# Performance work log

Measured on AMD Instinct MI355X. Metric: run time of the kernel, lower is better.

The kernel has to match this reference:

```python
import jax, jax.numpy as jnp
import numpy as np

N = 16384      # nodes
E = 524288     # edges (avg degree 32)
F_IN = 128     # input features
H1 = 256       # first_gcn_dimensions
H2 = 256       # second_gcn_dimensions
D1 = 64        # first_dense_neurons
D2 = 2         # second_dense_neurons (fixed by EYE=ones(2))


def setup_inputs() -> dict:
    key = jax.random.key(0)
    ks = jax.random.split(key, 8)
    w = lambda k, shp: (jax.random.normal(k, shp, jnp.float32) * 0.05)
    return dict(
        features=jax.random.normal(ks[0], (N, F_IN), jnp.float32),
        edges=jax.random.randint(ks[1], (2, E), 0, N),
        W1=w(ks[2], (F_IN, H1)), b1=jnp.zeros((H1,), jnp.float32),
        W2=w(ks[3], (H1, H2)), b2=jnp.zeros((H2,), jnp.float32),
        fc1_w=w(ks[4], (D1, H2)), fc1_b=jnp.zeros((D1,), jnp.float32),
        fc2_w=w(ks[5], (D2, D1)), fc2_b=jnp.zeros((D2,), jnp.float32),
    )


def gcn_conv(x, W, b, src, dst, n):
    """PyG GCNConv: xW, add self-loops, symmetric D^-1/2 (A+I) D^-1/2 aggregation."""
    x = x @ W
    loops = jnp.arange(n)
    s = jnp.concatenate([src, loops])
    d = jnp.concatenate([dst, loops])
    deg = jax.ops.segment_sum(jnp.ones(s.shape, x.dtype), d, num_segments=n)
    dinv = jnp.where(deg > 0, jax.lax.rsqrt(deg), 0.0)
    msg = x[s] * (dinv[s] * dinv[d])[:, None]          # gather + scale
    return jax.ops.segment_sum(msg, d, num_segments=n) + b  # scatter-add


def reference(features, edges, W1, b1, W2, b2, fc1_w, fc1_b, fc2_w, fc2_b):
    n = features.shape[0]
    src, dst = edges[0], edges[1]
    h1 = jax.nn.relu(gcn_conv(features, W1, b1, src, dst, n))
    h2 = gcn_conv(h1, W2, b2, src, dst, n)                 # [N, H2]
    a1 = jnp.tanh(h2 @ fc1_w.T + fc1_b)                    # [N, D1]
    assignment = jax.nn.softmax(a1 @ fc2_w.T + fc2_b, axis=1)  # [N, 2]
    group_features = assignment.T @ h2                     # [2, H2]
    # to_dense_adj: dense NxN adjacency, duplicate edges accumulate
    adj = jnp.zeros((n, n), h2.dtype).at[src, dst].add(1.0)
    new_adj = assignment.T @ (adj @ assignment)            # [2, 2]
    positive = jnp.clip(group_features[0][None, :], -100.0, 100.0)
    negative = jnp.clip(group_features[1][None, :], -100.0, 100.0)
    # F.normalize(p=1, dim=1) with eps=1e-12
    denom = jnp.maximum(jnp.sum(jnp.abs(new_adj), axis=1, keepdims=True), 1e-12)
    norm_diag = jnp.diag(new_adj / denom)
    pos_penalty = jnp.mean((norm_diag - 1.0) ** 2)         # MSE vs ones(2)
    graph_embedding = jnp.mean(group_features, axis=0, keepdims=True)  # [1, H2]
    return (graph_embedding, positive, negative, pos_penalty)
```

## Files before the change

### kernel.cpp

```cpp
#include <hip/hip_runtime.h>
#include <hip/hip_bf16.h>
#include <math.h>

#define N_NODES 16384
#define N_EDGES 524288
#define F_IN 128
#define H1 256
#define H2 256
#define D1 64
#define NA_GRID 128
#define DEG_CAP 96

typedef __attribute__((ext_vector_type(8))) short short8;
typedef __attribute__((ext_vector_type(4))) float floatx4;
typedef unsigned short ushort_t;
typedef unsigned int uint_t;

__device__ inline float bf2f(ushort_t u) {
    union { uint_t i; float f; } v;
    v.i = ((uint_t)u) << 16;
    return v.f;
}
__device__ inline ushort_t f2bs(float x) {
    __hip_bfloat16 h = __float2bfloat16(x);
    return *reinterpret_cast<ushort_t*>(&h);
}

__global__ __launch_bounds__(256) void prep_fill(
    const int* __restrict__ src, const int* __restrict__ dst,
    const float* __restrict__ features, const float* __restrict__ W1,
    const float* __restrict__ W2, const float* __restrict__ fc1_w,
    int* __restrict__ cur, int* __restrict__ col, ushort_t* __restrict__ z,
    ushort_t* __restrict__ W1t, ushort_t* __restrict__ W2t,
    ushort_t* __restrict__ fc1bf) {
    int b = blockIdx.x, t = threadIdx.x;
    if (b < 2048) {
        int e = b * 256 + t;
        int d = dst[e];
        int pos = atomicAdd(&cur[d], 1);
        if (pos < DEG_CAP) col[d * DEG_CAP + pos] = src[e];
    } else if (b < 4096) {
        int idx = ((b - 2048) * 256 + t) * 4;
        float4 v = *(const float4*)&features[idx];
        uint2 p;
        p.x = (uint_t)f2bs(v.x) | ((uint_t)f2bs(v.y) << 16);
        p.y = (uint_t)f2bs(v.z) | ((uint_t)f2bs(v.w) << 16);
        *(uint2*)&z[idx] = p;
    } else if (b < 4224) {
        int idx = (b - 4096) * 256 + t;
        int n = idx >> 7, k = idx & 127;
        W1t[idx] = f2bs(W1[k * 256 + n]);
    } else if (b < 4480) {
        int idx = (b - 4224) * 256 + t;
        int n = idx >> 8, k = idx & 255;
        W2t[idx] = f2bs(W2[k * 256 + n]);
    } else {
        int idx = (b - 4480) * 256 + t;
        fc1bf[idx] = f2bs(fc1_w[idx]);
    }
}

__global__ __launch_bounds__(256) void fused_layer1(
    const ushort_t* __restrict__ zfeat, const int* __restrict__ cnt,
    const int* __restrict__ col, const float* __restrict__ b1,
    const ushort_t* __restrict__ W1t, const ushort_t* __restrict__ W2t,
    ushort_t* __restrict__ bufY) {
    __shared__ __align__(16) ushort_t Az[16 * 136];
    __shared__ __align__(16) ushort_t Ah[16 * 264];
    const int tid = threadIdx.x;
    const int lane = tid & 63;
    const int wave = tid >> 6;
    const int m = lane & 15;
    const int quad = lane >> 4;
    const int row0 = blockIdx.x * 16;

    for (int ii = 0; ii < 4; ++ii) {
        const int nl = wave * 4 + ii;
        const int node = __builtin_amdgcn_readfirstlane(row0 + nl);
        const int foff = lane * 2;
        const int deg = cnt[node];
        float dnode = rsqrtf((float)(deg + 1));
        uint_t self = *(const uint_t*)&zfeat[(size_t)node * 128 + foff];
        float a0 = dnode * bf2f((ushort_t)(self & 0xffff));
        float a1 = dnode * bf2f((ushort_t)(self >> 16));
        const int s0 = node * DEG_CAP;
        const int s1 = s0 + min(deg, DEG_CAP);
        int base = s0;
        for (; base + 8 <= s1; base += 8) {
            uint_t uu[8]; float dv[8];
            #pragma unroll
            for (int q = 0; q < 8; ++q) {
                int j = col[base + q];
                dv[q] = rsqrtf((float)(cnt[j] + 1));
                uu[q] = *(const uint_t*)&zfeat[(size_t)j * 128 + foff];
            }
            #pragma unroll
            for (int q = 0; q < 8; ++q) {
                a0 += dv[q] * bf2f((ushort_t)(uu[q] & 0xffff));
                a1 += dv[q] * bf2f((ushort_t)(uu[q] >> 16));
            }
        }
        for (; base < s1; ++base) {
            int j = col[base];
            float dv = rsqrtf((float)(cnt[j] + 1));
            uint_t u = *(const uint_t*)&zfeat[(size_t)j * 128 + foff];
            a0 += dv * bf2f((ushort_t)(u & 0xffff));
            a1 += dv * bf2f((ushort_t)(u >> 16));
        }
        *(uint_t*)&Az[nl * 136 + foff] =
            (uint_t)f2bs(a0 * dnode) | ((uint_t)f2bs(a1 * dnode) << 16);
    }
    __syncthreads();

    const int wcol0 = wave * 64;
    floatx4 acc[4];
    const floatx4 zero4 = {0.f, 0.f, 0.f, 0.f};
    #pragma unroll
    for (int j = 0; j < 4; ++j) acc[j] = zero4;
    #pragma unroll
    for (int k0 = 0; k0 < 128; k0 += 32) {
        short8 a = *(const short8*)&Az[m * 136 + k0 + quad * 8];
        #pragma unroll
        for (int j = 0; j < 4; ++j) {
            short8 bb = *(const short8*)
                &W1t[(size_t)(wcol0 + j * 16 + m) * 128 + k0 + quad * 8];
            acc[j] = __builtin_amdgcn_mfma_f32_16x16x32_bf16(a, bb, acc[j], 0, 0, 0);
        }
    }
    #pragma unroll
    for (int j = 0; j < 4; ++j) {
        int cg = wcol0 + j * 16 + m;
        float bv = b1[cg];
        #pragma unroll
        for (int r = 0; r < 4; ++r) {
            float v = fmaxf(acc[j][r] + bv, 0.0f);
            Ah[(quad * 4 + r) * 264 + cg] = f2bs(v);
        }
    }
    __syncthreads();

    #pragma unroll
    for (int j = 0; j < 4; ++j) acc[j] = zero4;
    #pragma unroll
    for (int k0 = 0; k0 < 256; k0 += 32) {
        short8 a = *(const short8*)&Ah[m * 264 + k0 + quad * 8];
        #pragma unroll
        for (int j = 0; j < 4; ++j) {
            short8 bb = *(const short8*)
                &W2t[(size_t)(wcol0 + j * 16 + m) * 256 + k0 + quad * 8];
            acc[j] = __builtin_amdgcn_mfma_f32_16x16x32_bf16(a, bb, acc[j], 0, 0, 0);
        }
    }
    float rs4[4];
    #pragma unroll
    for (int r = 0; r < 4; ++r)
        rs4[r] = rsqrtf((float)(cnt[row0 + quad * 4 + r] + 1));
    #pragma unroll
    for (int j = 0; j < 4; ++j) {
        int cg = wcol0 + j * 16 + m;
        #pragma unroll
        for (int r = 0; r < 4; ++r)
            bufY[(size_t)(row0 + quad * 4 + r) * 256 + cg] = f2bs(acc[j][r] * rs4[r]);
    }
}

__global__ __launch_bounds__(256) void fused_assign(
    const ushort_t* __restrict__ bufY, const int* __restrict__ cnt,
    const int* __restrict__ col, const float* __restrict__ b2,
    const ushort_t* __restrict__ fc1bf, const float* __restrict__ fc1_b,
    const float* __restrict__ fc2_w, const float* __restrict__ fc2_b,
    float* __restrict__ assign, float* __restrict__ gfr) {
    __shared__ __align__(16) ushort_t Ah[16 * 264];
    __shared__ float sha[16][65];
    __shared__ float sas0[16], sas1[16];
    const int tid = threadIdx.x;
    const int lane = tid & 63;
    const int wave = tid >> 6;
    const int m = lane & 15;
    const int quad = lane >> 4;
    const int row0 = blockIdx.x * 16;

    for (int ii = 0; ii < 4; ++ii) {
        const int nl = wave * 4 + ii;
        const int node = __builtin_amdgcn_readfirstlane(row0 + nl);
        const int foff = lane * 4;
        const int deg = cnt[node];
        float a0, a1, a2, a3;
        {
            uint2 u = *(const uint2*)&bufY[(size_t)node * 256 + foff];
            a0 = bf2f((ushort_t)(u.x & 0xffff));
            a1 = bf2f((ushort_t)(u.x >> 16));
            a2 = bf2f((ushort_t)(u.y & 0xffff));
            a3 = bf2f((ushort_t)(u.y >> 16));
        }
        const int s0 = node * DEG_CAP;
        const int s1 = s0 + min(deg, DEG_CAP);
        int base = s0;
        for (; base + 8 <= s1; base += 8) {
            uint2 uu[8];
            #pragma unroll
            for (int q = 0; q < 8; ++q) {
                int j = col[base + q];
                uu[q] = *(const uint2*)&bufY[(size_t)j * 256 + foff];
            }
            #pragma unroll
            for (int q = 0; q < 8; ++q) {
                a0 += bf2f((ushort_t)(uu[q].x & 0xffff));
                a1 += bf2f((ushort_t)(uu[q].x >> 16));
                a2 += bf2f((ushort_t)(uu[q].y & 0xffff));
                a3 += bf2f((ushort_t)(uu[q].y >> 16));
            }
        }
        for (; base < s1; ++base) {
            int j = col[base];
            uint2 u = *(const uint2*)&bufY[(size_t)j * 256 + foff];
            a0 += bf2f((ushort_t)(u.x & 0xffff));
            a1 += bf2f((ushort_t)(u.x >> 16));
            a2 += bf2f((ushort_t)(u.y & 0xffff));
            a3 += bf2f((ushort_t)(u.y >> 16));
        }
        float di = rsqrtf((float)(deg + 1));
        uint2 pk;
        pk.x = (uint_t)f2bs(a0 * di + b2[foff + 0]) |
               ((uint_t)f2bs(a1 * di + b2[foff + 1]) << 16);
        pk.y = (uint_t)f2bs(a2 * di + b2[foff + 2]) |
               ((uint_t)f2bs(a3 * di + b2[foff + 3]) << 16);
        *(uint2*)&Ah[nl * 264 + foff] = pk;
    }
    __syncthreads();

    floatx4 acc = {0.f, 0.f, 0.f, 0.f};
    #pragma unroll
    for (int k0 = 0; k0 < 256; k0 += 32) {
        short8 a = *(const short8*)&Ah[m * 264 + k0 + quad * 8];
        short8 bb = *(const short8*)
            &fc1bf[(size_t)(wave * 16 + m) * 256 + k0 + quad * 8];
        acc = __builtin_amdgcn_mfma_f32_16x16x32_bf16(a, bb, acc, 0, 0, 0);
    }
    {
        int cg = wave * 16 + m;
        float bv = fc1_b[cg];
        #pragma unroll
        for (int r = 0; r < 4; ++r)
            sha[quad * 4 + r][cg] = tanhf(acc[r] + bv);
    }
    __syncthreads();

    if (tid < 16) {
        float p0 = fc2_b[0], p1 = fc2_b[1];
        #pragma unroll 8
        for (int t = 0; t < 64; ++t) {
            float a = sha[tid][t];
            p0 += a * fc2_w[t];
            p1 += a * fc2_w[64 + t];
        }
        float mx = fmaxf(p0, p1);
        float e0 = expf(p0 - mx), e1 = expf(p1 - mx);
        float inv = 1.0f / (e0 + e1);
        float2 as; as.x = e0 * inv; as.y = e1 * inv;
        *(float2*)&assign[(row0 + tid) * 2] = as;
        sas0[tid] = as.x; sas1[tid] = as.y;
    }
    __syncthreads();

    float acc0 = 0.f, acc1 = 0.f;
    #pragma unroll
    for (int i = 0; i < 16; ++i) {
        float h = bf2f(Ah[i * 264 + tid]);
        acc0 += sas0[i] * h;
        acc1 += sas1[i] * h;
    }
    float* gfc = gfr + (blockIdx.x & 3) * 512;
    atomicAdd(&gfc[tid], acc0);
    atomicAdd(&gfc[256 + tid], acc1);
}

__global__ __launch_bounds__(256) void newadj_fin(
    const int* __restrict__ src, const int* __restrict__ dst,
    const float* __restrict__ assign, float* __restrict__ napart,
    int* __restrict__ cntt, const float* __restrict__ gfr,
    float* __restrict__ out) {
    __shared__ float red[4][4];
    __shared__ int sticket;
    const int tid = threadIdx.x;
    const int b = blockIdx.x;
    const int lane = tid & 63;
    const int wave = tid >> 6;

    float a00 = 0.f, a01 = 0.f, a10 = 0.f, a11 = 0.f;
    for (int e = b * 256 + tid; e < N_EDGES; e += NA_GRID * 256) {
        int s = src[e], d = dst[e];
        float s0 = assign[s * 2], s1 = assign[s * 2 + 1];
        float d0 = assign[d * 2], d1 = assign[d * 2 + 1];
        a00 += s0 * d0; a01 += s0 * d1; a10 += s1 * d0; a11 += s1 * d1;
    }
    #pragma unroll
    for (int off = 32; off; off >>= 1) {
        a00 += __shfl_down(a00, off);
        a01 += __shfl_down(a01, off);
        a10 += __shfl_down(a10, off);
        a11 += __shfl_down(a11, off);
    }
    if (lane == 0) {
        red[wave][0] = a00; red[wave][1] = a01;
        red[wave][2] = a10; red[wave][3] = a11;
    }
    __syncthreads();
    if (tid < 4) {
        float v = red[0][tid] + red[1][tid] + red[2][tid] + red[3][tid];
        __hip_atomic_store(&napart[b * 4 + tid], v, __ATOMIC_RELEASE,
                           __HIP_MEMORY_SCOPE_AGENT);
    }
    __syncthreads();
    if (tid == 0)
        sticket = __hip_atomic_fetch_add(cntt, 1, __ATOMIC_ACQ_REL,
                                         __HIP_MEMORY_SCOPE_AGENT);
    __syncthreads();
    if (sticket != NA_GRID - 1) return;

    float acc = 0.f;
    for (int i = lane; i < NA_GRID; i += 64)
        acc += __hip_atomic_load(&napart[i * 4 + wave], __ATOMIC_RELAXED,
                                 __HIP_MEMORY_SCOPE_AGENT);
    #pragma unroll
    for (int off = 32; off; off >>= 1) acc += __shfl_down(acc, off);
    __shared__ float na[4];
    if (lane == 0) na[wave] = acc;
    __syncthreads();
    float g0 = gfr[tid] + gfr[512 + tid] + gfr[1024 + tid] + gfr[1536 + tid];
    float g1 = gfr[256 + tid] + gfr[768 + tid] + gfr[1280 + tid] + gfr[1792 + tid];
    out[tid] = 0.5f * (g0 + g1);
    out[256 + tid] = fminf(fmaxf(g0, -100.f), 100.f);
    out[512 + tid] = fminf(fmaxf(g1, -100.f), 100.f);
    if (tid == 0) {
        float n00 = na[0], n01 = na[1], n10 = na[2], n11 = na[3];
        float den0 = fmaxf(fabsf(n00) + fabsf(n01), 1e-12f);
        float den1 = fmaxf(fabsf(n10) + fabsf(n11), 1e-12f);
        float x0 = n00 / den0 - 1.0f;
        float x1 = n11 / den1 - 1.0f;
        out[768] = 0.5f * (x0 * x0 + x1 * x1);
    }
}


extern "C" void kernel_launch(void* const* d_in, const int* in_sizes, int n_in,
                              void* d_out, int out_size, void* d_ws, size_t ws_size,
                              hipStream_t stream) {
    const float* features = (const float*)d_in[0];
    const int* edges = (const int*)d_in[1];
    const int* src = edges;
    const int* dst = edges + N_EDGES;
    const float* W1 = (const float*)d_in[2];
    const float* b1 = (const float*)d_in[3];
    const float* W2 = (const float*)d_in[4];
    const float* b2 = (const float*)d_in[5];
    const float* fc1_w = (const float*)d_in[6];
    const float* fc1_b = (const float*)d_in[7];
    const float* fc2_w = (const float*)d_in[8];
    const float* fc2_b = (const float*)d_in[9];
    float* out = (float*)d_out;

    char* ws = (char*)d_ws;
    auto carve = [&](size_t bytes) {
        void* q = (void*)ws;
        ws += (bytes + 255) & ~(size_t)255;
        return q;
    };
    int* cur = (int*)carve(N_NODES * 4);
    float* gfr = (float*)carve(4 * 512 * 4);
    int* cnt_na = (int*)carve(256);
    int* col = (int*)carve((size_t)N_NODES * DEG_CAP * 4);
    float* assign = (float*)carve(N_NODES * 2 * 4);
    float* napart = (float*)carve(NA_GRID * 4 * 4);
    ushort_t* fc1bf = (ushort_t*)carve(64 * 256 * 2);
    ushort_t* zfeat = (ushort_t*)carve((size_t)N_NODES * F_IN * 2);
    ushort_t* W1t = (ushort_t*)carve(256 * 128 * 2);
    ushort_t* W2t = (ushort_t*)carve(256 * 256 * 2);
    ushort_t* bufY = (ushort_t*)carve((size_t)N_NODES * 256 * 2);

    hipMemsetAsync(cur, 0, N_NODES * 4 + 4 * 512 * 4 + 256, stream);

    prep_fill<<<4544, 256, 0, stream>>>(src, dst, features, W1, W2, fc1_w,
                                        cur, col, zfeat, W1t, W2t, fc1bf);
    fused_layer1<<<N_NODES / 16, 256, 0, stream>>>(
        zfeat, cur, col, b1, W1t, W2t, bufY);
    fused_assign<<<N_NODES / 16, 256, 0, stream>>>(
        bufY, cur, col, b2, fc1bf, fc1_b, fc2_w, fc2_b, assign, gfr);
    newadj_fin<<<NA_GRID, 256, 0, stream>>>(src, dst, assign, napart,
                                            cnt_na, gfr, out);
}
```

Measured before the change: 206.3 us.

## Pre-scale features by source degree and widen fused blocks to 512 threads

Adds a separate kernel that converts features to bf16 already multiplied by each node's D^-1/2, after degree counts are known. This removes the per-neighbor cnt[j] load and rsqrt from the layer-1 gather loop. Both fused kernels now run 512-thread blocks (8 waves, 2 nodes per wave), which halves the MFMA column tiles per wave, and the bf16 unpack uses a mask instead of a shift. The cost is an extra kernel launch and a serialization point: feature conversion can no longer overlap with the edge fill inside prep_fill.

After: 189.6 us. 8.1% less time.

```diff
diff --git a/kernel.cpp b/kernel.cpp
--- a/kernel.cpp
+++ b/kernel.cpp
@@ -21,6 +21,16 @@
     v.i = ((uint_t)u) << 16;
     return v.f;
 }
+__device__ inline float u2f_lo(uint_t u) {
+    union { uint_t i; float f; } v;
+    v.i = u << 16;
+    return v.f;
+}
+__device__ inline float u2f_hi(uint_t u) {
+    union { uint_t i; float f; } v;
+    v.i = u & 0xffff0000u;
+    return v.f;
+}
 __device__ inline ushort_t f2bs(float x) {
     __hip_bfloat16 h = __float2bfloat16(x);
     return *reinterpret_cast<ushort_t*>(&h);
@@ -28,9 +38,9 @@
 
 __global__ __launch_bounds__(256) void prep_fill(
     const int* __restrict__ src, const int* __restrict__ dst,
-    const float* __restrict__ features, const float* __restrict__ W1,
-    const float* __restrict__ W2, const float* __restrict__ fc1_w,
-    int* __restrict__ cur, int* __restrict__ col, ushort_t* __restrict__ z,
+    const float* __restrict__ W1, const float* __restrict__ W2,
+    const float* __restrict__ fc1_w,
+    int* __restrict__ cur, int* __restrict__ col,
     ushort_t* __restrict__ W1t, ushort_t* __restrict__ W2t,
     ushort_t* __restrict__ fc1bf) {
     int b = blockIdx.x, t = threadIdx.x;
@@ -39,29 +49,35 @@
         int d = dst[e];
         int pos = atomicAdd(&cur[d], 1);
         if (pos < DEG_CAP) col[d * DEG_CAP + pos] = src[e];
-    } else if (b < 4096) {
-        int idx = ((b - 2048) * 256 + t) * 4;
-        float4 v = *(const float4*)&features[idx];
-        uint2 p;
-        p.x = (uint_t)f2bs(v.x) | ((uint_t)f2bs(v.y) << 16);
-        p.y = (uint_t)f2bs(v.z) | ((uint_t)f2bs(v.w) << 16);
-        *(uint2*)&z[idx] = p;
-    } else if (b < 4224) {
-        int idx = (b - 4096) * 256 + t;
+    } else if (b < 2176) {
+        int idx = (b - 2048) * 256 + t;
         int n = idx >> 7, k = idx & 127;
         W1t[idx] = f2bs(W1[k * 256 + n]);
-    } else if (b < 4480) {
-        int idx = (b - 4224) * 256 + t;
+    } else if (b < 2432) {
+        int idx = (b - 2176) * 256 + t;
         int n = idx >> 8, k = idx & 255;
         W2t[idx] = f2bs(W2[k * 256 + n]);
     } else {
-        int idx = (b - 4480) * 256 + t;
+        int idx = (b - 2432) * 256 + t;
         fc1bf[idx] = f2bs(fc1_w[idx]);
     }
 }
 
-__global__ __launch_bounds__(256) void fused_layer1(
-    const ushort_t* __restrict__ zfeat, const int* __restrict__ cnt,
+__global__ __launch_bounds__(256) void scale_feat(
+    const float* __restrict__ features, const int* __restrict__ cnt,
+    ushort_t* __restrict__ zs) {
+    int gid = blockIdx.x * 256 + threadIdx.x;
+    int node = gid >> 5;
+    float d = rsqrtf((float)(cnt[node] + 1));
+    float4 v = *(const float4*)&features[gid * 4];
+    uint2 p;
+    p.x = (uint_t)f2bs(v.x * d) | ((uint_t)f2bs(v.y * d) << 16);
+    p.y = (uint_t)f2bs(v.z * d) | ((uint_t)f2bs(v.w * d) << 16);
+    *(uint2*)&zs[gid * 4] = p;
+}
+
+__global__ __launch_bounds__(512, 8) void fused_layer1(
+    const ushort_t* __restrict__ zs, const int* __restrict__ cnt,
     const int* __restrict__ col, const float* __restrict__ b1,
     const ushort_t* __restrict__ W1t, const ushort_t* __restrict__ W2t,
     ushort_t* __restrict__ bufY) {
@@ -74,61 +90,58 @@
     const int quad = lane >> 4;
     const int row0 = blockIdx.x * 16;
 
-    for (int ii = 0; ii < 4; ++ii) {
-        const int nl = wave * 4 + ii;
+    for (int ii = 0; ii < 2; ++ii) {
+        const int nl = wave * 2 + ii;
         const int node = __builtin_amdgcn_readfirstlane(row0 + nl);
         const int foff = lane * 2;
-        const int deg = cnt[node];
-        float dnode = rsqrtf((float)(deg + 1));
-        uint_t self = *(const uint_t*)&zfeat[(size_t)node * 128 + foff];
-        float a0 = dnode * bf2f((ushort_t)(self & 0xffff));
-        float a1 = dnode * bf2f((ushort_t)(self >> 16));
+        const int deg = __builtin_amdgcn_readfirstlane(cnt[node]);
+        uint_t self = *(const uint_t*)&zs[(size_t)node * 128 + foff];
+        float a0 = u2f_lo(self);
+        float a1 = u2f_hi(self);
         const int s0 = node * DEG_CAP;
         const int s1 = s0 + min(deg, DEG_CAP);
         int base = s0;
         for (; base + 8 <= s1; base += 8) {
-            uint_t uu[8]; float dv[8];
+            uint_t uu[8];
             #pragma unroll
             for (int q = 0; q < 8; ++q) {
                 int j = col[base + q];
-                dv[q] = rsqrtf((float)(cnt[j] + 1));
-                uu[q] = *(const uint_t*)&zfeat[(size_t)j * 128 + foff];
+                uu[q] = *(const uint_t*)&zs[(size_t)j * 128 + foff];
             }
             #pragma unroll
             for (int q = 0; q < 8; ++q) {
-                a0 += dv[q] * bf2f((ushort_t)(uu[q] & 0xffff));
-                a1 += dv[q] * bf2f((ushort_t)(uu[q] >> 16));
+                a0 += u2f_lo(uu[q]);
+                a1 += u2f_hi(uu[q]);
             }
         }
         for (; base < s1; ++base) {
             int j = col[base];
-            float dv = rsqrtf((float)(cnt[j] + 1));
-            uint_t u = *(const uint_t*)&zfeat[(size_t)j * 128 + foff];
-            a0 += dv * bf2f((ushort_t)(u & 0xffff));
-            a1 += dv * bf2f((ushort_t)(u >> 16));
-        }
+            uint_t u = *(const uint_t*)&zs[(size_t)j * 128 + foff];
+            a0 += u2f_lo(u);
+            a1 += u2f_hi(u);
+        }
+        float dnode = rsqrtf((float)(deg + 1));
         *(uint_t*)&Az[nl * 136 + foff] =
             (uint_t)f2bs(a0 * dnode) | ((uint_t)f2bs(a1 * dnode) << 16);
     }
     __syncthreads();
 
-    const int wcol0 = wave * 64;
-    floatx4 acc[4];
+    const int wcol0 = wave * 32;
+    floatx4 acc[2];
     const floatx4 zero4 = {0.f, 0.f, 0.f, 0.f};
-    #pragma unroll
-    for (int j = 0; j < 4; ++j) acc[j] = zero4;
+    acc[0] = zero4; acc[1] = zero4;
     #pragma unroll
     for (int k0 = 0; k0 < 128; k0 += 32) {
         short8 a = *(const short8*)&Az[m * 136 + k0 + quad * 8];
         #pragma unroll
-        for (int j = 0; j < 4; ++j) {
+        for (int j = 0; j < 2; ++j) {
             short8 bb = *(const short8*)
                 &W1t[(size_t)(wcol0 + j * 16 + m) * 128 + k0 + quad * 8];
             acc[j] = __builtin_amdgcn_mfma_f32_16x16x32_bf16(a, bb, acc[j], 0, 0, 0);
         }
     }
     #pragma unroll
-    for (int j = 0; j < 4; ++j) {
+    for (int j = 0; j < 2; ++j) {
         int cg = wcol0 + j * 16 + m;
         float bv = b1[cg];
         #pragma unroll
@@ -139,13 +152,12 @@
     }
     __syncthreads();
 
-    #pragma unroll
-    for (int j = 0; j < 4; ++j) acc[j] = zero4;
+    acc[0] = zero4; acc[1] = zero4;
     #pragma unroll
     for (int k0 = 0; k0 < 256; k0 += 32) {
         short8 a = *(const short8*)&Ah[m * 264 + k0 + quad * 8];
         #pragma unroll
-        for (int j = 0; j < 4; ++j) {
+        for (int j = 0; j < 2; ++j) {
             short8 bb = *(const short8*)
                 &W2t[(size_t)(wcol0 + j * 16 + m) * 256 + k0 + quad * 8];
             acc[j] = __builtin_amdgcn_mfma_f32_16x16x32_bf16(a, bb, acc[j], 0, 0, 0);
@@ -156,7 +168,7 @@
     for (int r = 0; r < 4; ++r)
         rs4[r] = rsqrtf((float)(cnt[row0 + quad * 4 + r] + 1));
     #pragma unroll
-    for (int j = 0; j < 4; ++j) {
+    for (int j = 0; j < 2; ++j) {
         int cg = wcol0 + j * 16 + m;
         #pragma unroll
         for (int r = 0; r < 4; ++r)
@@ -164,7 +176,7 @@
     }
 }
 
-__global__ __launch_bounds__(256) void fused_assign(
+__global__ __launch_bounds__(512, 8) void fused_assign(
     const ushort_t* __restrict__ bufY, const int* __restrict__ cnt,
     const int* __restrict__ col, const float* __restrict__ b2,
     const ushort_t* __restrict__ fc1bf, const float* __restrict__ fc1_b,
@@ -180,18 +192,16 @@
     const int quad = lane >> 4;
     const int row0 = blockIdx.x * 16;
 
-    for (int ii = 0; ii < 4; ++ii) {
-        const int nl = wave * 4 + ii;
+    for (int ii = 0; ii < 2; ++ii) {
+        const int nl = wave * 2 + ii;
         const int node = __builtin_amdgcn_readfirstlane(row0 + nl);
         const int foff = lane * 4;
-        const int deg = cnt[node];
+        const int deg = __builtin_amdgcn_readfirstlane(cnt[node]);
         float a0, a1, a2, a3;
         {
             uint2 u = *(const uint2*)&bufY[(size_t)node * 256 + foff];
-            a0 = bf2f((ushort_t)(u.x & 0xffff));
-            a1 = bf2f((ushort_t)(u.x >> 16));
-            a2 = bf2f((ushort_t)(u.y & 0xffff));
-            a3 = bf2f((ushort_t)(u.y >> 16));
+            a0 = u2f_lo(u.x); a1 = u2f_hi(u.x);
+            a2 = u2f_lo(u.y); a3 = u2f_hi(u.y);
         }
         const int s0 = node * DEG_CAP;
         const int s1 = s0 + min(deg, DEG_CAP);
@@ -205,19 +215,15 @@
             }
             #pragma unroll
             for (int q = 0; q < 8; ++q) {
-                a0 += bf2f((ushort_t)(uu[q].x & 0xffff));
-                a1 += bf2f((ushort_t)(uu[q].x >> 16));
-                a2 += bf2f((ushort_t)(uu[q].y & 0xffff));
-                a3 += bf2f((ushort_t)(uu[q].y >> 16));
+                a0 += u2f_lo(uu[q].x); a1 += u2f_hi(uu[q].x);
+                a2 += u2f_lo(uu[q].y); a3 += u2f_hi(uu[q].y);
             }
         }
         for (; base < s1; ++base) {
             int j = col[base];
             uint2 u = *(const uint2*)&bufY[(size_t)j * 256 + foff];
-            a0 += bf2f((ushort_t)(u.x & 0xffff));
-            a1 += bf2f((ushort_t)(u.x >> 16));
-            a2 += bf2f((ushort_t)(u.y & 0xffff));
-            a3 += bf2f((ushort_t)(u.y >> 16));
+            a0 += u2f_lo(u.x); a1 += u2f_hi(u.x);
+            a2 += u2f_lo(u.y); a3 += u2f_hi(u.y);
         }
         float di = rsqrtf((float)(deg + 1));
         uint2 pk;
@@ -229,15 +235,15 @@
     }
     __syncthreads();
 
-    floatx4 acc = {0.f, 0.f, 0.f, 0.f};
-    #pragma unroll
-    for (int k0 = 0; k0 < 256; k0 += 32) {
-        short8 a = *(const short8*)&Ah[m * 264 + k0 + quad * 8];
-        short8 bb = *(const short8*)
-            &fc1bf[(size_t)(wave * 16 + m) * 256 + k0 + quad * 8];
-        acc = __builtin_amdgcn_mfma_f32_16x16x32_bf16(a, bb, acc, 0, 0, 0);
-    }
-    {
+    if (wave < 4) {
+        floatx4 acc = {0.f, 0.f, 0.f, 0.f};
+        #pragma unroll
+        for (int k0 = 0; k0 < 256; k0 += 32) {
+            short8 a = *(const short8*)&Ah[m * 264 + k0 + quad * 8];
+            short8 bb = *(const short8*)
+                &fc1bf[(size_t)(wave * 16 + m) * 256 + k0 + quad * 8];
+            acc = __builtin_amdgcn_mfma_f32_16x16x32_bf16(a, bb, acc, 0, 0, 0);
+        }
         int cg = wave * 16 + m;
         float bv = fc1_b[cg];
         #pragma unroll
@@ -263,16 +269,17 @@
     }
     __syncthreads();
 
-    float acc0 = 0.f, acc1 = 0.f;
-    #pragma unroll
-    for (int i = 0; i < 16; ++i) {
-        float h = bf2f(Ah[i * 264 + tid]);
-        acc0 += sas0[i] * h;
-        acc1 += sas1[i] * h;
-    }
-    float* gfc = gfr + (blockIdx.x & 3) * 512;
-    atomicAdd(&gfc[tid], acc0);
-    atomicAdd(&gfc[256 + tid], acc1);
+    {
+        const int f = tid & 255;
+        const int which = tid >> 8;
+        const float* sv = which ? sas1 : sas0;
+        float acc = 0.f;
+        #pragma unroll
+        for (int i = 0; i < 16; ++i)
+            acc += sv[i] * bf2f(Ah[i * 264 + f]);
+        float* gfc = gfr + (blockIdx.x & 3) * 512;
+        atomicAdd(&gfc[which * 256 + f], acc);
+    }
 }
 
 __global__ __launch_bounds__(256) void newadj_fin(
@@ -373,18 +380,19 @@
     float* assign = (float*)carve(N_NODES * 2 * 4);
     float* napart = (float*)carve(NA_GRID * 4 * 4);
     ushort_t* fc1bf = (ushort_t*)carve(64 * 256 * 2);
-    ushort_t* zfeat = (ushort_t*)carve((size_t)N_NODES * F_IN * 2);
+    ushort_t* zs = (ushort_t*)carve((size_t)N_NODES * F_IN * 2);
     ushort_t* W1t = (ushort_t*)carve(256 * 128 * 2);
     ushort_t* W2t = (ushort_t*)carve(256 * 256 * 2);
     ushort_t* bufY = (ushort_t*)carve((size_t)N_NODES * 256 * 2);
 
     hipMemsetAsync(cur, 0, N_NODES * 4 + 4 * 512 * 4 + 256, stream);
 
-    prep_fill<<<4544, 256, 0, stream>>>(src, dst, features, W1, W2, fc1_w,
-                                        cur, col, zfeat, W1t, W2t, fc1bf);
-    fused_layer1<<<N_NODES / 16, 256, 0, stream>>>(
-        zfeat, cur, col, b1, W1t, W2t, bufY);
-    fused_assign<<<N_NODES / 16, 256, 0, stream>>>(
+    prep_fill<<<2496, 256, 0, stream>>>(src, dst, W1, W2, fc1_w,
+                                        cur, col, W1t, W2t, fc1bf);
+    scale_feat<<<2048, 256, 0, stream>>>(features, cur, zs);
+    fused_layer1<<<N_NODES / 16, 512, 0, stream>>>(
+        zs, cur, col, b1, W1t, W2t, bufY);
+    fused_assign<<<N_NODES / 16, 512, 0, stream>>>(
         bufY, cur, col, b2, fc1bf, fc1_b, fc2_w, fc2_b, assign, gfr);
     newadj_fin<<<NA_GRID, 256, 0, stream>>>(src, dst, assign, napart,
                                             cnt_na, gfr, out);
```
